# Performance work log

Measured on AMD Instinct MI355X. Metric: run time of the kernel, lower is better.

## Reference

```python
import jax, jax.numpy as jnp
import numpy as np

EPS = 1e-3  # eps in grad_pursuit_update_step


def _grad_pursuit(signal, dictionary, target_l0):
    """signal: [B, V], dictionary: [F, V] -> dense weights [B, F] (nonneg)."""
    B, V = signal.shape
    F = dictionary.shape[0]
    rows = jnp.arange(B)

    def step(weights, _):
        # residual = signal - weights @ D         [B, V]
        residual = signal - jnp.einsum('bf,fv->bv', weights, dictionary)
        # inner products with every atom          [B, F]
        inner = jnp.einsum('bv,fv->bf', residual, dictionary)
        idx = jnp.argmax(inner, axis=1)           # [B]
        selected = (weights != 0).at[rows, idx].set(True)
        grad = jnp.where(selected, inner, jnp.zeros((), signal.dtype))  # [B, F]
        c = jnp.einsum('bf,fv->bv', grad, dictionary)                   # [B, V]
        c_sq = jnp.sum(c * c, axis=-1)
        step_size = jnp.sum(c * residual, axis=-1) / jnp.maximum(c_sq, EPS)
        weights = jax.nn.relu(weights + step_size[:, None] * grad)
        return weights, None

    w0 = jnp.zeros((B, F), dtype=signal.dtype)
    weights, _ = jax.lax.scan(step, w0, None, length=target_l0)
    return weights


def _decode(indices, weights, dictionary):
    # embedding-bag sum: gather rows then weighted sum over k
    return jnp.einsum('bk,bkv->bv', weights, dictionary[indices])


def setup_inputs() -> dict:
    key = jax.random.key(0)
    k1, k2, k3, k4, k5 = jax.random.split(key, 5)
    B, D, F = 1024, 1024, 8192
    x = jax.random.normal(k1, (B, D), dtype=jnp.float32)
    y = jax.random.normal(k2, (B, D), dtype=jnp.float32)
    xs = jax.random.normal(k3, (F, D), dtype=jnp.float32)
    xs = xs / jnp.linalg.norm(xs, axis=-1, keepdims=True)  # module stores unit-norm atoms
    ys = jax.random.normal(k4, (F, D), dtype=jnp.float32)
    ys = ys / jnp.linalg.norm(jax.random.normal(k3, (F, D)), axis=-1, keepdims=True)
    mean_y = 0.1 * jax.random.normal(k5, (D,), dtype=jnp.float32)
    return {"x": x, "y": y, "xs": xs, "ys": ys, "mean_y": mean_y, "target_l0": 16}


def reference(x, y, xs, ys, mean_y, target_l0):
    # ITDA.forward with subtract_mean=False, skip_connection=False, fvu_loss=True
    dense = _grad_pursuit(x, xs, target_l0)               # [B, F]
    weights, indices = jax.lax.top_k(dense, target_l0)    # [B, k], [B, k]
    x_rec = _decode(indices, weights, xs)                  # [B, V]
    y_rec = _decode(indices, weights, ys)                  # [B, V]
    l2 = jnp.sum((y - y_rec) ** 2, axis=-1)                # [B]
    total_var = jnp.mean(jnp.sum((y - mean_y) ** 2, axis=-1))
    losses = l2 / total_var
    return weights, indices, x_rec, y_rec, losses
```

## Files before the change

### kernel.cpp

```cpp
#include <hip/hip_runtime.h>
#include <cstdint>
#include <cstddef>

#define B_N 1024
#define V_N 1024
#define F_N 8192
#define NSEL 16
#define NITER 16
#define EPSV 1e-3f
#define WINF 0.008f
#define CANDMAX 64
#define CAND2 256
#define NTILE 64

#define BM 64
#define BN 128
#define BK 32
#define NBN (F_N / BN)

typedef __attribute__((ext_vector_type(4))) float f32x4;
typedef __attribute__((ext_vector_type(8))) short bf16x8;
typedef unsigned short u16;
typedef unsigned char u8;

#define GLDS16(g, l) __builtin_amdgcn_global_load_lds((__attribute__((address_space(1))) void*)(g), (__attribute__((address_space(3))) void*)(l), 16, 0, 0)

__device__ __forceinline__ u16 f2bf(float f) {
  unsigned u = __float_as_uint(f);
  return (u16)((u + 0x7FFFu + ((u >> 16) & 1u)) >> 16);
}

__device__ __forceinline__ float block_sum256(float v, float* sbuf) {
#pragma unroll
  for (int o = 32; o > 0; o >>= 1) v += __shfl_down(v, o, 64);
  int lane = threadIdx.x & 63, wid = threadIdx.x >> 6;
  if (lane == 0) sbuf[wid] = v;
  __syncthreads();
  float r = sbuf[0] + sbuf[1] + sbuf[2] + sbuf[3];
  __syncthreads();
  return r;
}

__device__ __forceinline__ float block_max256(float v, float* sbuf) {
#pragma unroll
  for (int o = 32; o > 0; o >>= 1) v = fmaxf(v, __shfl_down(v, o, 64));
  int lane = threadIdx.x & 63, wid = threadIdx.x >> 6;
  if (lane == 0) sbuf[wid] = v;
  __syncthreads();
  float r = fmaxf(fmaxf(sbuf[0], sbuf[1]), fmaxf(sbuf[2], sbuf[3]));
  __syncthreads();
  return r;
}

__device__ __forceinline__ float wave_tree64(float v) {
#pragma unroll
  for (int o = 32; o > 0; o >>= 1) v += __shfl_down(v, o, 64);
  return v;
}

__device__ __forceinline__ float seq_dot(const float* __restrict__ xrow,
                                         const float* __restrict__ sr) {
  float acc = 0.f;
  for (int k = 0; k < V_N; k += 4) {
    float4 xv = *(const float4*)(xrow + k);
    acc = __builtin_fmaf(xv.x, sr[k + 0], acc);
    acc = __builtin_fmaf(xv.y, sr[k + 1], acc);
    acc = __builtin_fmaf(xv.z, sr[k + 2], acc);
    acc = __builtin_fmaf(xv.w, sr[k + 3], acc);
  }
  return acc;
}

__device__ __forceinline__ void wave_g(const float* __restrict__ xr,
                                       const float* __restrict__ sr,
                                       int lane, float* __restrict__ out) {
  float part[4];
#pragma unroll
  for (int vw = 0; vw < 4; vw++) {
    int vt = vw * 64 + lane;
    float4 xvv = *(const float4*)(xr + vt * 4);
    float4 rl4 = *(const float4*)&sr[vt * 4];
    float p = xvv.x * rl4.x + xvv.y * rl4.y + xvv.z * rl4.z + xvv.w * rl4.w;
    part[vw] = wave_tree64(p);
  }
  if (lane == 0) *out = part[0] + part[1] + part[2] + part[3];
}

__global__ __launch_bounds__(256) void rowvar_kernel(const float* __restrict__ y,
                                                     const float* __restrict__ mean_y,
                                                     float* __restrict__ rowvar,
                                                     int* __restrict__ act_cnt) {
  int b = blockIdx.x, t = threadIdx.x;
  __shared__ float sred[4];
  float4 yv = *(const float4*)(y + (size_t)b * V_N + t * 4);
  float4 mv = *(const float4*)(mean_y + t * 4);
  float dx = yv.x - mv.x, dy = yv.y - mv.y, dz = yv.z - mv.z, dw = yv.w - mv.w;
  float p = dx * dx + dy * dy + dz * dz + dw * dw;
  float s = block_sum256(p, sred);
  if (t == 0) { rowvar[b] = s; act_cnt[b] = 0; }
}

__global__ __launch_bounds__(256) void reduce_var_kernel(const float* __restrict__ rowvar,
                                                         float* __restrict__ totvar) {
  __shared__ float sred[4];
  int t = threadIdx.x;
  float p = 0.f;
#pragma unroll
  for (int i = 0; i < 4; i++) p += rowvar[t * 4 + i];
  float s = block_sum256(p, sred);
  if (t == 0) totvar[0] = s / (float)B_N;
}

__global__ __launch_bounds__(256) void xh_kernel(const float* __restrict__ xs,
                                                 u16* __restrict__ Xh) {
  int b = blockIdx.x, t = threadIdx.x;
  float4 v = *(const float4*)(xs + (size_t)b * V_N + t * 4);
  u16* o = Xh + (size_t)b * V_N + t * 4;
  o[0] = f2bf(v.x); o[1] = f2bf(v.y); o[2] = f2bf(v.z); o[3] = f2bf(v.w);
}

__global__ __launch_bounds__(256) void init_kernel(const float* __restrict__ x,
                                                   float* __restrict__ R,
                                                   u16* __restrict__ Rh,
                                                   float* __restrict__ rn2) {
  int b = blockIdx.x, t = threadIdx.x;
  __shared__ float sred[4];
  float4 v = *(const float4*)(x + (size_t)b * V_N + t * 4);
  *(float4*)(R + (size_t)b * V_N + t * 4) = v;
  u16* o = Rh + (size_t)b * V_N + t * 4;
  o[0] = f2bf(v.x); o[1] = f2bf(v.y); o[2] = f2bf(v.z); o[3] = f2bf(v.w);
  float p = v.x * v.x + v.y * v.y + v.z * v.z + v.w * v.w;
  float s = block_sum256(p, sred);
  if (t == 0) rn2[b] = s;
}

__global__ __launch_bounds__(256) void gemm_scan_kernel(const u16* __restrict__ Rh,
                                                        const u16* __restrict__ Xh,
                                                        const float* __restrict__ rn2,
                                                        u8* __restrict__ inner8,
                                                        float* __restrict__ pval) {
  __shared__ u16 As[128 * 32];
  __shared__ u16 Bs[128 * 32];
  __shared__ float srmax[128][2];
  const int tid = threadIdx.x;
  const int w = tid >> 6, l = tid & 63;
  const int flat = blockIdx.y * 64 + blockIdx.x;
  const int wg = (flat & 7) * 64 + (flat >> 3);
  const int bn = wg & 63, bm = wg >> 6;
  const int wr = w >> 1, wc = w & 1;
  const int lr = l & 15, lg = l >> 4;

  f32x4 acc[4][4];
#pragma unroll
  for (int m = 0; m < 4; m++)
#pragma unroll
    for (int n = 0; n < 4; n++) acc[m][n] = (f32x4){0.f, 0.f, 0.f, 0.f};

  const u16* Ab = Rh + (size_t)bm * 128 * V_N;
  const u16* Bb = Xh + (size_t)bn * 128 * V_N;
  const int srow = w * 16 + (l >> 2);
  const int scol = (l & 3) * 8;

  for (int k0 = 0; k0 < V_N; k0 += 32) {
#pragma unroll
    for (int i = 0; i < 2; i++) {
      GLDS16(Ab + (size_t)(i * 64 + srow) * V_N + k0 + scol, As + i * 2048 + w * 512);
      GLDS16(Bb + (size_t)(i * 64 + srow) * V_N + k0 + scol, Bs + i * 2048 + w * 512);
    }
    __syncthreads();
    bf16x8 af[4], bfr[4];
#pragma unroll
    for (int m = 0; m < 4; m++) af[m] = *(const bf16x8*)&As[(wr * 64 + m * 16 + lr) * 32 + lg * 8];
#pragma unroll
    for (int n = 0; n < 4; n++) bfr[n] = *(const bf16x8*)&Bs[(wc * 64 + n * 16 + lr) * 32 + lg * 8];
#pragma unroll
    for (int m = 0; m < 4; m++)
#pragma unroll
      for (int n = 0; n < 4; n++)
        acc[m][n] = __builtin_amdgcn_mfma_f32_16x16x32_bf16(af[m], bfr[n], acc[m][n], 0, 0, 0);
    __syncthreads();
  }

#pragma unroll
  for (int m = 0; m < 4; m++) {
#pragma unroll
    for (int j = 0; j < 4; j++) {
      float pm = acc[m][0][j];
#pragma unroll
      for (int n = 1; n < 4; n++) pm = fmaxf(pm, acc[m][n][j]);
#pragma unroll
      for (int mk = 1; mk < 16; mk <<= 1) pm = fmaxf(pm, __shfl_xor(pm, mk, 64));
      if (lr == 0) srmax[wr * 64 + m * 16 + lg * 4 + j][wc] = pm;
    }
  }
  __syncthreads();
  if (tid < 128) {
    float v = fmaxf(srmax[tid][0], srmax[tid][1]);
    pval[(size_t)(bm * 128 + tid) * NTILE + bn] = v;
  }
#pragma unroll
  for (int m = 0; m < 4; m++) {
#pragma unroll
    for (int j = 0; j < 4; j++) {
      int row = wr * 64 + m * 16 + lg * 4 + j;
      float rmax = fmaxf(srmax[row][0], srmax[row][1]);
      float qinv = 250.0f / fmaxf(WINF * sqrtf(rn2[bm * 128 + row]), 1e-20f);
      int gm = bm * 128 + row;
#pragma unroll
      for (int n = 0; n < 4; n++) {
        int gn = bn * 128 + wc * 64 + n * 16 + lr;
        float df = floorf((rmax - acc[m][n][j]) * qinv);
        int u = df >= 254.f ? 254 : (int)df;
        inner8[(size_t)gm * F_N + gn] = (u8)u;
      }
    }
  }
}

__global__ __launch_bounds__(256, 4) void scan_update_kernel(const float* __restrict__ x,
                                                             const float* __restrict__ xs,
                                                             const u8* __restrict__ inner8,
                                                             const float* __restrict__ pval,
                                                             float* __restrict__ rn2,
                                                             int* __restrict__ act_ids,
                                                             float* __restrict__ act_w,
                                                             int* __restrict__ act_cnt,
                                                             float* __restrict__ R,
                                                             u16* __restrict__ Rh) {
  int b = blockIdx.x, t = threadIdx.x;
  const int lane = t & 63, wid = t >> 6;
  __shared__ float sr[V_N];
  __shared__ float spv[NTILE];
  __shared__ int   shot[NTILE];
  __shared__ int   snhot;
  __shared__ float sred[4];
  __shared__ float smax[4];
  __shared__ float scsqp[4], scrp[4];
  __shared__ int   scand[CAND2];
  __shared__ float scval[CAND2];
  __shared__ float sfv[256];
  __shared__ int   sfi[256];
  __shared__ int   scnt_c;
  __shared__ int   sbii;
  __shared__ float sg[NSEL + 2];
  __shared__ float sw[NSEL + 2];
  __shared__ int   sids[NSEL + 2];
  __shared__ int   ssel[NSEL + 2];
  __shared__ int   scnt, scnt0, sjnew;

  float4 rv = *(const float4*)(R + (size_t)b * V_N + t * 4);
  float4 xrow = *(const float4*)(x + (size_t)b * V_N + t * 4);
  *(float4*)&sr[t * 4] = rv;
  if (t < NTILE) spv[t] = pval[(size_t)b * NTILE + t];
  if (t == 0) {
    scnt_c = 0; snhot = 0;
    int c0 = act_cnt[b]; scnt0 = c0;
    for (int j = 0; j < c0; j++) { sids[j] = act_ids[b * NSEL + j]; sw[j] = act_w[b * NSEL + j]; }
  }
  __syncthreads();

  float M = block_max256(spv[t & (NTILE - 1)], smax);
  float win = WINF * sqrtf(rn2[b]);
  float thr = M - win;
  float qinv = 250.0f / fmaxf(win, 1e-20f);

  if (t < NTILE && spv[t] >= thr) { int p = atomicAdd(&snhot, 1); shot[p] = t; }
  __syncthreads();
  int nh = snhot;
  const u8* irow8 = inner8 + (size_t)b * F_N;
  for (int h = 0; h < nh; h += 2) {
    int hh = h + (t >> 7);
    if (hh < nh) {
      int tt = shot[hh];
      int lim = (int)floorf((spv[tt] - thr) * qinv);
      int u8v = irow8[tt * 128 + (t & 127)];
      if (u8v <= lim) { int p = atomicAdd(&scnt_c, 1); if (p < CAND2) scand[p] = tt * 128 + (t & 127); }
    }
  }
  __syncthreads();
  int total = scnt_c;
  int cnt0 = scnt0;

  if (wid >= 1) {
#pragma unroll
    for (int jj = 0; jj < 6; jj++) {
      int j = (wid - 1) + 3 * jj;
      if (j < cnt0 && sw[j] != 0.f)
        wave_g(xs + (size_t)sids[j] * V_N, sr, lane, &sg[j]);
    }
  } else if (total <= CANDMAX) {
    int nc = total;
    if (nc == 1) {
      if (lane == 0) sbii = scand[0];
    } else {
      if (lane < nc) scval[lane] = seq_dot(xs + (size_t)scand[lane] * V_N, sr);
      if (lane == 0) {
        float bv = scval[0]; int bi = scand[0];
        for (int c = 1; c < nc; c++) {
          float v = scval[c]; int id = scand[c];
          if (v > bv || (v == bv && id < bi)) { bv = v; bi = id; }
        }
        sbii = bi;
      }
    }
  }
  __syncthreads();

  if (total > CANDMAX && total <= CAND2) {
    if (t < total) scval[t] = seq_dot(xs + (size_t)scand[t] * V_N, sr);
    __syncthreads();
    if (t == 0) {
      float bv = scval[0]; int bi = scand[0];
      for (int c = 1; c < total; c++) {
        float v = scval[c]; int id = scand[c];
        if (v > bv || (v == bv && id < bi)) { bv = v; bi = id; }
      }
      sbii = bi;
    }
    __syncthreads();
  } else if (total > CAND2) {
    float bv = -1e30f; int bi = 0x7fffffff;
    for (int f = t; f < F_N; f += 256) {
      float acc = seq_dot(xs + (size_t)f * V_N, sr);
      if (acc > bv) { bv = acc; bi = f; }
    }
    sfv[t] = bv; sfi[t] = bi;
    __syncthreads();
    if (t == 0) {
      float bbv = sfv[0]; int bbi = sfi[0];
      for (int c = 1; c < 256; c++) {
        float v = sfv[c]; int id = sfi[c];
        if (v > bbv || (v == bbv && id < bbi)) { bbv = v; bbi = id; }
      }
      sbii = bbi;
    }
    __syncthreads();
  }

  if (t == 0) {
    int bi = sbii;
    int cnt = cnt0;
    int pos = -1;
    for (int j = 0; j < cnt; j++) if (sids[j] == bi) pos = j;
    if (pos < 0) { pos = cnt; sids[cnt] = bi; sw[cnt] = 0.f; cnt++; }
    for (int j = 0; j < cnt; j++) ssel[j] = (sw[j] != 0.f) || (j == pos) ? 1 : 0;
    for (int j = 0; j < cnt; j++) if (!ssel[j]) sg[j] = 0.f;
    sjnew = (sw[pos] == 0.f) ? pos : -1;
    scnt = cnt;
  }
  __syncthreads();
  int cnt = scnt;

  int jnew = sjnew;
  if (jnew >= 0 && wid == 0)
    wave_g(xs + (size_t)sids[jnew] * V_N, sr, lane, &sg[jnew]);
  __syncthreads();

  float4 rl = *(const float4*)&sr[t * 4];
  float4 xv[NSEL + 1];
#pragma unroll
  for (int j = 0; j < NSEL + 1; j++) {
    int jj = j < cnt ? j : 0;
    xv[j] = *(const float4*)(xs + (size_t)sids[jj] * V_N + t * 4);
  }

  float4 cv = {0.f, 0.f, 0.f, 0.f};
#pragma unroll
  for (int j = 0; j < NSEL + 1; j++) {
    if (j < cnt) {
      if (ssel[j]) {
        float g = sg[j];
        cv.x += g * xv[j].x; cv.y += g * xv[j].y; cv.z += g * xv[j].z; cv.w += g * xv[j].w;
      }
    }
  }
  float pcsq = cv.x * cv.x + cv.y * cv.y + cv.z * cv.z + cv.w * cv.w;
  float pcr  = cv.x * rl.x + cv.y * rl.y + cv.z * rl.z + cv.w * rl.w;
  {
    float s1 = wave_tree64(pcsq);
    float s2 = wave_tree64(pcr);
    if (lane == 0) { scsqp[wid] = s1; scrp[wid] = s2; }
  }
  __syncthreads();

  if (t == 0) {
    float csq = scsqp[0] + scsqp[1] + scsqp[2] + scsqp[3];
    float cr  = scrp[0] + scrp[1] + scrp[2] + scrp[3];
    float step = cr / fmaxf(csq, EPSV);
    for (int j = 0; j < cnt; j++)
      if (ssel[j]) sw[j] = fmaxf(sw[j] + step * sg[j], 0.f);
    for (int j = 0; j < cnt; j++) {
      act_ids[b * NSEL + j] = sids[j];
      act_w[b * NSEL + j] = sw[j];
    }
    act_cnt[b] = cnt;
  }
  __syncthreads();

  float4 r = xrow;
#pragma unroll
  for (int j = 0; j < NSEL + 1; j++) {
    if (j < cnt) {
      float wv = sw[j];
      if (wv != 0.f) {
        r.x -= wv * xv[j].x; r.y -= wv * xv[j].y; r.z -= wv * xv[j].z; r.w -= wv * xv[j].w;
      }
    }
  }
  *(float4*)(R + (size_t)b * V_N + t * 4) = r;
  u16* o = Rh + (size_t)b * V_N + t * 4;
  o[0] = f2bf(r.x); o[1] = f2bf(r.y); o[2] = f2bf(r.z); o[3] = f2bf(r.w);
  float p2 = r.x * r.x + r.y * r.y + r.z * r.z + r.w * r.w;
  float s2 = block_sum256(p2, sred);
  if (t == 0) rn2[b] = s2;
}

__global__ __launch_bounds__(256) void residual_kernel(const float* __restrict__ x,
                                                       const float* __restrict__ xs,
                                                       const int* __restrict__ act_ids,
                                                       const float* __restrict__ act_w,
                                                       const int* __restrict__ act_cnt,
                                                       float* __restrict__ R) {
  int b = blockIdx.x, t = threadIdx.x;
  float4 r = *(const float4*)(x + (size_t)b * V_N + t * 4);
  int cnt = act_cnt[b];
  for (int j = 0; j < cnt; j++) {
    float w = act_w[b * NSEL + j];
    if (w != 0.f) {
      const float* xr = xs + (size_t)act_ids[b * NSEL + j] * V_N;
      float4 xv = *(const float4*)(xr + t * 4);
      r.x -= w * xv.x; r.y -= w * xv.y; r.z -= w * xv.z; r.w -= w * xv.w;
    }
  }
  *(float4*)(R + (size_t)b * V_N + t * 4) = r;
}

__global__ __launch_bounds__(256) void gemm_argmax_kernel(const float* __restrict__ R,
                                                          const float* __restrict__ xs,
                                                          float* __restrict__ pval,
                                                          int* __restrict__ pidx) {
  __shared__ float sA[BK * 68];
  __shared__ float sB[BK * 132];
  __shared__ float sMv[64 * 33];
  __shared__ int   sMi[64 * 33];

  int tid = threadIdx.x;
  int bn = blockIdx.x, bm = blockIdx.y;
  float acc[8][4];
#pragma unroll
  for (int i = 0; i < 8; i++)
#pragma unroll
    for (int j = 0; j < 4; j++) acc[i][j] = 0.f;

  int r0 = (tid >> 5) << 3;
  int n0 = (tid & 31) << 2;
  const float* Rbase = R + (size_t)(bm * BM) * V_N;
  const float* Xbase = xs + (size_t)(bn * BN) * V_N;

  for (int k0 = 0; k0 < V_N; k0 += BK) {
    {
      int m = tid >> 2, kf = (tid & 3) * 4;
      float4 v = *(const float4*)(Rbase + (size_t)m * V_N + k0 + kf);
      sA[(kf + 0) * 68 + m] = v.x; sA[(kf + 1) * 68 + m] = v.y;
      sA[(kf + 2) * 68 + m] = v.z; sA[(kf + 3) * 68 + m] = v.w;
      float4 v2 = *(const float4*)(Rbase + (size_t)m * V_N + k0 + kf + 16);
      sA[(kf + 16) * 68 + m] = v2.x; sA[(kf + 17) * 68 + m] = v2.y;
      sA[(kf + 18) * 68 + m] = v2.z; sA[(kf + 19) * 68 + m] = v2.w;
    }
    {
      int nn = tid >> 3, kf = (tid & 7) * 4;
#pragma unroll
      for (int i = 0; i < 4; i++) {
        int n = nn + i * 32;
        float4 v = *(const float4*)(Xbase + (size_t)n * V_N + k0 + kf);
        sB[(kf + 0) * 132 + n] = v.x; sB[(kf + 1) * 132 + n] = v.y;
        sB[(kf + 2) * 132 + n] = v.z; sB[(kf + 3) * 132 + n] = v.w;
      }
    }
    __syncthreads();
#pragma unroll
    for (int k = 0; k < BK; k++) {
      float4 aL = *(float4*)&sA[k * 68 + r0];
      float4 aH = *(float4*)&sA[k * 68 + r0 + 4];
      float4 bv = *(float4*)&sB[k * 132 + n0];
      float a[8] = {aL.x, aL.y, aL.z, aL.w, aH.x, aH.y, aH.z, aH.w};
      float bb[4] = {bv.x, bv.y, bv.z, bv.w};
#pragma unroll
      for (int i = 0; i < 8; i++)
#pragma unroll
        for (int j = 0; j < 4; j++) acc[i][j] += a[i] * bb[j];
    }
    __syncthreads();
  }

#pragma unroll
  for (int i = 0; i < 8; i++) {
    float bvv = acc[i][0]; int bj = 0;
#pragma unroll
    for (int j = 1; j < 4; j++)
      if (acc[i][j] > bvv) { bvv = acc[i][j]; bj = j; }
    sMv[(r0 + i) * 33 + (tid & 31)] = bvv;
    sMi[(r0 + i) * 33 + (tid & 31)] = bn * BN + n0 + bj;
  }
  __syncthreads();
  if (tid < 64) {
    float bvv = sMv[tid * 33]; int bi = sMi[tid * 33];
    for (int c = 1; c < 32; c++) {
      float v = sMv[tid * 33 + c];
      if (v > bvv) { bvv = v; bi = sMi[tid * 33 + c]; }
    }
    pval[(size_t)(bm * BM + tid) * NBN + bn] = bvv;
    pidx[(size_t)(bm * BM + tid) * NBN + bn] = bi;
  }
}

__global__ __launch_bounds__(256) void combine_update_kernel(const float* __restrict__ R,
                                                             const float* __restrict__ xs,
                                                             const float* __restrict__ pval,
                                                             const int* __restrict__ pidx,
                                                             int* __restrict__ act_ids,
                                                             float* __restrict__ act_w,
                                                             int* __restrict__ act_cnt) {
  int b = blockIdx.x, t = threadIdx.x;
  __shared__ float sr[V_N];
  __shared__ float sred[4];
  __shared__ float sg[NSEL + 1];
  __shared__ float sw[NSEL + 1];
  __shared__ int   sids[NSEL + 1];
  __shared__ int   ssel[NSEL + 1];
  __shared__ int   scnt;

  float4 rv = *(const float4*)(R + (size_t)b * V_N + t * 4);
  *(float4*)&sr[t * 4] = rv;

  if (t == 0) {
    const float* pv = pval + (size_t)b * NBN;
    const int* pi = pidx + (size_t)b * NBN;
    float bv = pv[0]; int bi = pi[0];
    for (int c = 1; c < NBN; c++) {
      float v = pv[c];
      if (v > bv) { bv = v; bi = pi[c]; }
    }
    int cnt = act_cnt[b];
    for (int j = 0; j < cnt; j++) { sids[j] = act_ids[b * NSEL + j]; sw[j] = act_w[b * NSEL + j]; }
    int pos = -1;
    for (int j = 0; j < cnt; j++) if (sids[j] == bi) pos = j;
    if (pos < 0) { pos = cnt; sids[cnt] = bi; sw[cnt] = 0.f; cnt++; }
    for (int j = 0; j < cnt; j++) ssel[j] = (sw[j] != 0.f) || (j == pos) ? 1 : 0;
    scnt = cnt;
  }
  __syncthreads();
  int cnt = scnt;

  for (int j = 0; j < cnt; j++) {
    if (!ssel[j]) { if (t == 0) sg[j] = 0.f; continue; }
    const float* xr = xs + (size_t)sids[j] * V_N;
    float4 xv = *(const float4*)(xr + t * 4);
    float4 rl = *(const float4*)&sr[t * 4];
    float p = xv.x * rl.x + xv.y * rl.y + xv.z * rl.z + xv.w * rl.w;
    float s = block_sum256(p, sred);
    if (t == 0) sg[j] = s;
  }
  __syncthreads();

  float4 cv = {0.f, 0.f, 0.f, 0.f};
  for (int j = 0; j < cnt; j++) {
    if (ssel[j]) {
      float g = sg[j];
      const float* xr = xs + (size_t)sids[j] * V_N;
      float4 xv = *(const float4*)(xr + t * 4);
      cv.x += g * xv.x; cv.y += g * xv.y; cv.z += g * xv.z; cv.w += g * xv.w;
    }
  }
  float4 rl = *(const float4*)&sr[t * 4];
  float pcsq = cv.x * cv.x + cv.y * cv.y + cv.z * cv.z + cv.w * cv.w;
  float pcr  = cv.x * rl.x + cv.y * rl.y + cv.z * rl.z + cv.w * rl.w;
  float csq = block_sum256(pcsq, sred);
  float cr  = block_sum256(pcr, sred);

  if (t == 0) {
    float step = cr / fmaxf(csq, EPSV);
    for (int j = 0; j < cnt; j++)
      if (ssel[j]) sw[j] = fmaxf(sw[j] + step * sg[j], 0.f);
    for (int j = 0; j < cnt; j++) {
      act_ids[b * NSEL + j] = sids[j];
      act_w[b * NSEL + j] = sw[j];
    }
    act_cnt[b] = cnt;
  }
}

__global__ __launch_bounds__(256) void topk_kernel(const int* __restrict__ act_ids,
                                                   const float* __restrict__ act_w,
                                                   const int* __restrict__ act_cnt,
                                                   float* __restrict__ out_w,
                                                   float* __restrict__ out_i) {
  int b = blockIdx.x * blockDim.x + threadIdx.x;
  if (b >= B_N) return;
  int cnt = act_cnt[b];
  int ids[NSEL]; float w[NSEL]; int m = 0;
  for (int j = 0; j < cnt; j++) {
    float wv = act_w[b * NSEL + j];
    if (wv > 0.f) { ids[m] = act_ids[b * NSEL + j]; w[m] = wv; m++; }
  }
  for (int i = 1; i < m; i++) {
    float wv = w[i]; int id = ids[i]; int j = i - 1;
    while (j >= 0 && (w[j] < wv || (w[j] == wv && ids[j] > id))) {
      w[j + 1] = w[j]; ids[j + 1] = ids[j]; j--;
    }
    w[j + 1] = wv; ids[j + 1] = id;
  }
  int nf = 0;
  for (int s = m; s < NSEL; s++) {
    for (;;) {
      bool used = false;
      for (int j = 0; j < m; j++) if (ids[j] == nf) used = true;
      if (!used) break;
      nf++;
    }
    ids[s] = nf; w[s] = 0.f; nf++;
  }
  for (int s = 0; s < NSEL; s++) {
    out_w[b * NSEL + s] = w[s];
    out_i[b * NSEL + s] = (float)ids[s];
  }
}

__global__ __launch_bounds__(256) void decode_kernel(const float* __restrict__ y,
                                                     const float* __restrict__ xs,
                                                     const float* __restrict__ ys,
                                                     const float* __restrict__ out_w,
                                                     const float* __restrict__ out_i,
                                                     const float* __restrict__ totvar,
                                                     float* __restrict__ x_rec,
                                                     float* __restrict__ y_rec,
                                                     float* __restrict__ losses) {
  int b = blockIdx.x, t = threadIdx.x;
  __shared__ float swv[NSEL];
  __shared__ int sid[NSEL];
  __shared__ float sred[4];
  if (t < NSEL) { swv[t] = out_w[b * NSEL + t]; sid[t] = (int)out_i[b * NSEL + t]; }
  __syncthreads();
  float4 xr = {0.f, 0.f, 0.f, 0.f}, yr = {0.f, 0.f, 0.f, 0.f};
  for (int s = 0; s < NSEL; s++) {
    float wv = swv[s];
    if (wv != 0.f) {
      const float* xrow = xs + (size_t)sid[s] * V_N;
      const float* yrow = ys + (size_t)sid[s] * V_N;
      float4 a = *(const float4*)(xrow + t * 4);
      float4 c = *(const float4*)(yrow + t * 4);
      xr.x += wv * a.x; xr.y += wv * a.y; xr.z += wv * a.z; xr.w += wv * a.w;
      yr.x += wv * c.x; yr.y += wv * c.y; yr.z += wv * c.z; yr.w += wv * c.w;
    }
  }
  *(float4*)(x_rec + (size_t)b * V_N + t * 4) = xr;
  *(float4*)(y_rec + (size_t)b * V_N + t * 4) = yr;
  float4 yv = *(const float4*)(y + (size_t)b * V_N + t * 4);
  float dx = yv.x - yr.x, dy = yv.y - yr.y, dz = yv.z - yr.z, dw = yv.w - yr.w;
  float p = dx * dx + dy * dy + dz * dz + dw * dw;
  float l2 = block_sum256(p, sred);
  if (t == 0) losses[b] = l2 / totvar[0];
}

extern "C" void kernel_launch(void* const* d_in, const int* in_sizes, int n_in,
                              void* d_out, int out_size, void* d_ws, size_t ws_size,
                              hipStream_t stream) {
  const float* x      = (const float*)d_in[0];
  const float* y      = (const float*)d_in[1];
  const float* xs     = (const float*)d_in[2];
  const float* ys     = (const float*)d_in[3];
  const float* mean_y = (const float*)d_in[4];
  (void)in_sizes; (void)n_in; (void)out_size;

  float* out    = (float*)d_out;
  float* out_w  = out;
  float* out_i  = out + 16384;
  float* out_xr = out + 32768;
  float* out_yr = out + 32768 + 1048576;
  float* out_ls = out + 32768 + 2097152;

  float* ws = (float*)d_ws;

  const size_t FAST_NEED = (size_t)14257153 * 4;

  if (ws_size >= FAST_NEED) {
    float* R      = ws;
    u8*    inner8 = (u8*)(ws + 1048576);
    u16*   Rh     = (u16*)(ws + 9437184);
    u16*   Xh     = (u16*)(ws + 9961472);
    float* rn2    = ws + 14155776;
    int*   aid    = (int*)(ws + 14156800);
    float* aw     = ws + 14173184;
    int*   acn    = (int*)(ws + 14189568);
    float* rv     = ws + 14190592;
    float* tv     = ws + 14191616;
    float* pval   = ws + 14191617;

    rowvar_kernel<<<B_N, 256, 0, stream>>>(y, mean_y, rv, acn);
    reduce_var_kernel<<<1, 256, 0, stream>>>(rv, tv);
    xh_kernel<<<F_N, 256, 0, stream>>>(xs, Xh);
    init_kernel<<<B_N, 256, 0, stream>>>(x, R, Rh, rn2);

    for (int it = 0; it < NITER; it++) {
      gemm_scan_kernel<<<dim3(F_N / 128, B_N / 128), 256, 0, stream>>>(Rh, Xh, rn2, inner8, pval);
      scan_update_kernel<<<B_N, 256, 0, stream>>>(x, xs, inner8, pval, rn2, aid, aw, acn, R, Rh);
    }

    topk_kernel<<<(B_N + 255) / 256, 256, 0, stream>>>(aid, aw, acn, out_w, out_i);
    decode_kernel<<<B_N, 256, 0, stream>>>(y, xs, ys, out_w, out_i, tv, out_xr, out_yr, out_ls);
  } else {
    float* R    = ws;
    float* pval = ws + 1048576;
    int*   pidx = (int*)(ws + 1114112);
    int*   aid  = (int*)(ws + 1179648);
    float* aw   = ws + 1196032;
    int*   acn  = (int*)(ws + 1212416);
    float* rv   = ws + 1213440;
    float* tv   = ws + 1214464;

    rowvar_kernel<<<B_N, 256, 0, stream>>>(y, mean_y, rv, acn);
    reduce_var_kernel<<<1, 256, 0, stream>>>(rv, tv);

    for (int it = 0; it < NITER; it++) {
      residual_kernel<<<B_N, 256, 0, stream>>>(x, xs, aid, aw, acn, R);
      gemm_argmax_kernel<<<dim3(NBN, B_N / BM), 256, 0, stream>>>(R, xs, pval, pidx);
      combine_update_kernel<<<B_N, 256, 0, stream>>>(R, xs, pval, pidx, aid, aw, acn);
    }

    topk_kernel<<<(B_N + 255) / 256, 256, 0, stream>>>(aid, aw, acn, out_w, out_i);
    decode_kernel<<<B_N, 256, 0, stream>>>(y, xs, ys, out_w, out_i, tv, out_xr, out_yr, out_ls);
  }
}
```

Measured before the change: 1.105 ms.

## Pack quantized inner-product bytes into 32-bit stores and precompute per-row scale

The GEMM epilogue now packs four 8-bit quantized inner products into one 32-bit store instead of four scattered byte stores, and the scan kernel remaps the permuted column order back to the true atom index. The per-row quantization scale is computed once in the init and update kernels and stored in a new buffer, so the GEMM epilogue no longer does a sqrt and divide per row. The workgroup swizzle is removed in favour of direct blockIdx mapping, which may change L2 reuse. The workspace layout is compacted to match.

New measurement: 1.031 ms. 1.07x faster.

```diff
diff --git a/kernel.cpp b/kernel.cpp
--- a/kernel.cpp
+++ b/kernel.cpp
@@ -122,7 +122,8 @@
 __global__ __launch_bounds__(256) void init_kernel(const float* __restrict__ x,
                                                    float* __restrict__ R,
                                                    u16* __restrict__ Rh,
-                                                   float* __restrict__ rn2) {
+                                                   float* __restrict__ rn2,
+                                                   float* __restrict__ qv) {
   int b = blockIdx.x, t = threadIdx.x;
   __shared__ float sred[4];
   float4 v = *(const float4*)(x + (size_t)b * V_N + t * 4);
@@ -131,12 +132,15 @@
   o[0] = f2bf(v.x); o[1] = f2bf(v.y); o[2] = f2bf(v.z); o[3] = f2bf(v.w);
   float p = v.x * v.x + v.y * v.y + v.z * v.z + v.w * v.w;
   float s = block_sum256(p, sred);
-  if (t == 0) rn2[b] = s;
+  if (t == 0) {
+    rn2[b] = s;
+    qv[b] = 250.0f / fmaxf(WINF * sqrtf(s), 1e-20f);
+  }
 }
 
 __global__ __launch_bounds__(256) void gemm_scan_kernel(const u16* __restrict__ Rh,
                                                         const u16* __restrict__ Xh,
-                                                        const float* __restrict__ rn2,
+                                                        const float* __restrict__ qv,
                                                         u8* __restrict__ inner8,
                                                         float* __restrict__ pval) {
   __shared__ u16 As[128 * 32];
@@ -144,9 +148,7 @@
   __shared__ float srmax[128][2];
   const int tid = threadIdx.x;
   const int w = tid >> 6, l = tid & 63;
-  const int flat = blockIdx.y * 64 + blockIdx.x;
-  const int wg = (flat & 7) * 64 + (flat >> 3);
-  const int bn = wg & 63, bm = wg >> 6;
+  const int bn = blockIdx.x, bm = blockIdx.y;
   const int wr = w >> 1, wc = w & 1;
   const int lr = l & 15, lg = l >> 4;
 
@@ -203,16 +205,17 @@
 #pragma unroll
     for (int j = 0; j < 4; j++) {
       int row = wr * 64 + m * 16 + lg * 4 + j;
+      int gm = bm * 128 + row;
       float rmax = fmaxf(srmax[row][0], srmax[row][1]);
-      float qinv = 250.0f / fmaxf(WINF * sqrtf(rn2[bm * 128 + row]), 1e-20f);
-      int gm = bm * 128 + row;
+      float qinv = qv[gm];
+      unsigned pack = 0;
 #pragma unroll
       for (int n = 0; n < 4; n++) {
-        int gn = bn * 128 + wc * 64 + n * 16 + lr;
         float df = floorf((rmax - acc[m][n][j]) * qinv);
-        int u = df >= 254.f ? 254 : (int)df;
-        inner8[(size_t)gm * F_N + gn] = (u8)u;
+        unsigned u = df >= 254.f ? 254u : (unsigned)(int)df;
+        pack |= u << (8 * n);
       }
+      *(unsigned*)(inner8 + (size_t)gm * F_N + bn * 128 + wc * 64 + lr * 4) = pack;
     }
   }
 }
@@ -222,6 +225,7 @@
                                                              const u8* __restrict__ inner8,
                                                              const float* __restrict__ pval,
                                                              float* __restrict__ rn2,
+                                                             float* __restrict__ qv,
                                                              int* __restrict__ act_ids,
                                                              float* __restrict__ act_w,
                                                              int* __restrict__ act_cnt,
@@ -273,8 +277,12 @@
     if (hh < nh) {
       int tt = shot[hh];
       int lim = (int)floorf((spv[tt] - thr) * qinv);
-      int u8v = irow8[tt * 128 + (t & 127)];
-      if (u8v <= lim) { int p = atomicAdd(&scnt_c, 1); if (p < CAND2) scand[p] = tt * 128 + (t & 127); }
+      int p = t & 127;
+      int u8v = irow8[tt * 128 + p];
+      if (u8v <= lim) {
+        int col = (p & 64) + (p & 3) * 16 + ((p >> 2) & 15);
+        int q = atomicAdd(&scnt_c, 1); if (q < CAND2) scand[q] = tt * 128 + col;
+      }
     }
   }
   __syncthreads();
@@ -412,7 +420,10 @@
   o[0] = f2bf(r.x); o[1] = f2bf(r.y); o[2] = f2bf(r.z); o[3] = f2bf(r.w);
   float p2 = r.x * r.x + r.y * r.y + r.z * r.z + r.w * r.w;
   float s2 = block_sum256(p2, sred);
-  if (t == 0) rn2[b] = s2;
+  if (t == 0) {
+    rn2[b] = s2;
+    qv[b] = 250.0f / fmaxf(WINF * sqrtf(s2), 1e-20f);
+  }
 }
 
 __global__ __launch_bounds__(256) void residual_kernel(const float* __restrict__ x,
@@ -681,29 +692,30 @@
 
   float* ws = (float*)d_ws;
 
-  const size_t FAST_NEED = (size_t)14257153 * 4;
+  const size_t FAST_NEED = (size_t)14258177 * 4;
 
   if (ws_size >= FAST_NEED) {
     float* R      = ws;
     u8*    inner8 = (u8*)(ws + 1048576);
-    u16*   Rh     = (u16*)(ws + 9437184);
-    u16*   Xh     = (u16*)(ws + 9961472);
-    float* rn2    = ws + 14155776;
-    int*   aid    = (int*)(ws + 14156800);
-    float* aw     = ws + 14173184;
-    int*   acn    = (int*)(ws + 14189568);
-    float* rv     = ws + 14190592;
-    float* tv     = ws + 14191616;
+    u16*   Rh     = (u16*)(ws + 5242880);
+    u16*   Xh     = (u16*)(ws + 5767168);
+    float* rn2    = ws + 9961472;
+    int*   aid    = (int*)(ws + 9962496);
+    float* aw     = ws + 9978880;
+    int*   acn    = (int*)(ws + 9995264);
+    float* rv     = ws + 9996288;
+    float* tv     = ws + 9997312;
     float* pval   = ws + 14191617;
+    float* qv     = ws + 14257153;
 
     rowvar_kernel<<<B_N, 256, 0, stream>>>(y, mean_y, rv, acn);
     reduce_var_kernel<<<1, 256, 0, stream>>>(rv, tv);
     xh_kernel<<<F_N, 256, 0, stream>>>(xs, Xh);
-    init_kernel<<<B_N, 256, 0, stream>>>(x, R, Rh, rn2);
+    init_kernel<<<B_N, 256, 0, stream>>>(x, R, Rh, rn2, qv);
 
     for (int it = 0; it < NITER; it++) {
-      gemm_scan_kernel<<<dim3(F_N / 128, B_N / 128), 256, 0, stream>>>(Rh, Xh, rn2, inner8, pval);
-      scan_update_kernel<<<B_N, 256, 0, stream>>>(x, xs, inner8, pval, rn2, aid, aw, acn, R, Rh);
+      gemm_scan_kernel<<<dim3(F_N / 128, B_N / 128), 256, 0, stream>>>(Rh, Xh, qv, inner8, pval);
+      scan_update_kernel<<<B_N, 256, 0, stream>>>(x, xs, inner8, pval, rn2, qv, aid, aw, acn, R, Rh);
     }
 
     topk_kernel<<<(B_N + 255) / 256, 256, 0, stream>>>(aid, aw, acn, out_w, out_i);
```
